# Kernel tuning notes

Measured on AMD Instinct MI355X. Metric: run time of the kernel, lower is better.

## Reference

```python
import jax, jax.numpy as jnp
import numpy as np

N = 131072      # points (rays x samples chunk)
E = 8           # spatial sub-networks (centroids)
DIN = 90        # encoded pos+dir features fed to sub-NeRFs (xyz_real=True -> x[:, 3:])
H = 256         # sub-NeRF hidden width
DOUT = 4        # rgb + sigma
MARGIN = 2.0    # boundary_margin
EPS = 1e-8


def setup_inputs() -> dict:
    key = jax.random.key(0)
    k = jax.random.split(key, 5)
    x_xyz = jax.random.uniform(k[0], (N, 3), dtype=jnp.float32)          # routing coords in [0,1)^3
    x_feat = jax.random.normal(k[1], (N, DIN), dtype=jnp.float32)        # encoded features
    x = jnp.concatenate([x_xyz, x_feat], axis=1)                         # [N, 3+DIN]
    centroids = jax.random.uniform(k[2], (E, 3), dtype=jnp.float32)
    W1 = jax.random.normal(k[3], (E, DIN, H), dtype=jnp.float32) * 0.05
    b1 = jnp.zeros((E, H), dtype=jnp.float32)
    W2 = jax.random.normal(k[4], (E, H, DOUT), dtype=jnp.float32) * 0.05
    b2 = jnp.zeros((E, DOUT), dtype=jnp.float32)
    return {"x": x, "centroids": centroids, "W1": W1, "b1": b1, "W2": W2, "b2": b2}


def reference(x, centroids, W1, b1, W2, b2):
    # --- centroid routing (torch.cdist equivalent) ---
    xyz = x[:, :3]                                                       # [N,3]
    d2 = jnp.sum((xyz[:, None, :] - centroids[None, :, :]) ** 2, axis=-1)
    dist = jnp.sqrt(jnp.maximum(d2, 0.0))                                # [N,E]
    inv = 1.0 / (dist + EPS)
    min_d = jnp.min(dist, axis=1, keepdims=True)                         # [N,1]
    inv = jnp.where(dist > MARGIN * min_d, 0.0, inv)                     # zero far experts
    weights = inv / jnp.sum(inv, axis=-1, keepdims=True)                 # [N,E], rows sum to 1

    # --- per-expert sub-NeRF MLP, weighted combine ---
    # Dense-equivalent of masked gather + weighted scatter-add: experts whose
    # weight is exactly 0 contribute nothing, matching the torch masked path.
    feat = x[:, 3:]                                                      # xyz_real=True -> drop xyz
    h = jax.nn.relu(jnp.einsum('nd,edh->enh', feat, W1) + b1[:, None, :])  # [E,N,H]
    out_e = jnp.einsum('enh,eho->eno', h, W2) + b2[:, None, :]             # [E,N,DOUT]
    return jnp.einsum('eno,ne->no', out_e, weights)                        # [N,DOUT]
```

## Files before the change

### kernel.cpp

```cpp
#include <hip/hip_runtime.h>

#define NPTS 131072
#define NE 8
#define DIN 90
#define NH 256

typedef __attribute__((ext_vector_type(8))) short bf16x8;
typedef __attribute__((ext_vector_type(4))) float f32x4;
typedef __attribute__((ext_vector_type(2))) float f32x2;
typedef __attribute__((ext_vector_type(4))) unsigned int u32x4;
typedef __attribute__((ext_vector_type(2))) unsigned int u32x2;
typedef __attribute__((ext_vector_type(4), aligned(4))) float f32x4a;
typedef __attribute__((ext_vector_type(2), aligned(4))) float f32x2a;

__device__ __forceinline__ unsigned short f2bf(float f) {
  unsigned int u = __float_as_uint(f);
  u += 0x7fffu + ((u >> 16) & 1u);
  return (unsigned short)(u >> 16);
}

#if defined(__has_builtin) && __has_builtin(__builtin_amdgcn_cvt_pk_bf16_f32)
typedef __attribute__((ext_vector_type(2))) __bf16 bf16x2;
__device__ __forceinline__ unsigned int pkbf(float f0, float f1) {
  bf16x2 r = __builtin_amdgcn_cvt_pk_bf16_f32(f0, f1);
  return __builtin_bit_cast(unsigned int, r);
}
#else
__device__ __forceinline__ unsigned int pkbf(float f0, float f1) {
  unsigned int u0 = __float_as_uint(f0) + 0x7fffu;
  unsigned int u1 = __float_as_uint(f1) + 0x7fffu;
  return __builtin_amdgcn_perm(u1, u0, 0x07060302u);
}
#endif

__device__ __forceinline__ bf16x8 cvt8(f32x4 a, f32x4 b) {
  u32x4 r;
  r[0] = pkbf(a[0], a[1]);
  r[1] = pkbf(a[2], a[3]);
  r[2] = pkbf(b[0], b[1]);
  r[3] = pkbf(b[2], b[3]);
  return __builtin_bit_cast(bf16x8, r);
}

__global__ __launch_bounds__(256) void prep(const float* __restrict__ W1,
                                            const float* __restrict__ W2,
                                            unsigned short* __restrict__ W1T,
                                            unsigned short* __restrict__ W2T) {
  const int t = threadIdx.x;
  if (blockIdx.x < 32) {
    const int e = blockIdx.x >> 2;
    const int n0 = (blockIdx.x & 3) * 64;
    __shared__ unsigned int ld[64][49];
    const int nl = t & 63;
    const int kq = t >> 6;
#pragma unroll
    for (int j = 0; j < 12; ++j) {
      const int kp2 = kq + 4 * j;
      const int k0 = 2 * kp2, k1 = k0 + 1;
      unsigned int lo = 0, hi = 0;
      if (k0 < DIN) lo = f2bf(W1[((size_t)e * DIN + k0) * NH + n0 + nl]);
      if (k1 < DIN) hi = f2bf(W1[((size_t)e * DIN + k1) * NH + n0 + nl]);
      ld[nl][kp2] = lo | (hi << 16);
    }
    __syncthreads();
    unsigned int* dst = (unsigned int*)(W1T + (size_t)(e * NH + n0) * 96);
#pragma unroll
    for (int j = 0; j < 12; ++j) {
      const int u = t + 256 * j;
      dst[u] = ld[u / 48][u % 48];
    }
  } else {
    const int e = blockIdx.x - 32;
    unsigned int* dst = (unsigned int*)W2T + (size_t)e * 2048;
    const float* src = W2 + (size_t)e * 1024;
#pragma unroll
    for (int j = 0; j < 8; ++j) {
      const int u = t + 256 * j;
      const int o = u >> 7;
      const int kp = u & 127;
      unsigned int v = 0;
      if (o < 4) {
        unsigned int lo = f2bf(src[(2 * kp) * 4 + o]);
        unsigned int hi = f2bf(src[(2 * kp + 1) * 4 + o]);
        v = lo | (hi << 16);
      }
      dst[u] = v;
    }
  }
}

__global__ __launch_bounds__(256, 3) void meganerf_main(
    const float* __restrict__ x, const float* __restrict__ cent,
    const float* __restrict__ b1, const float* __restrict__ b2,
    const unsigned short* __restrict__ W1T, const unsigned short* __restrict__ W2T,
    float* __restrict__ out) {
  __shared__ unsigned short sH[4 * 2048];
  __shared__ float sW[NE][64];
  __shared__ float sB2[64][4];
  __shared__ float sB1[NE * NH];

  const int t    = threadIdx.x;
  const int lane = t & 63;
  const int wid  = t >> 6;
  const int l15  = lane & 15;
  const int l4   = lane >> 4;
  const int row0 = blockIdx.x * 64;
  const int gbase = wid * 2048;

#pragma unroll
  for (int j = 0; j < 2; ++j)
    *(f32x4*)&sB1[t * 4 + j * 1024] = *(const f32x4a*)&b1[t * 4 + j * 1024];

  bf16x8 bfr[4][3];
#pragma unroll
  for (int nf = 0; nf < 4; ++nf) {
    const float* gr = x + (size_t)(row0 + 16 * nf + l15) * 93 + 3;
    f32x4 v0, v1;
    v0 = *(const f32x4a*)(gr + 8 * l4);
    v1 = *(const f32x4a*)(gr + 8 * l4 + 4);
    bfr[nf][0] = cvt8(v0, v1);
    v0 = *(const f32x4a*)(gr + 32 + 8 * l4);
    v1 = *(const f32x4a*)(gr + 36 + 8 * l4);
    bfr[nf][1] = cvt8(v0, v1);
    if (l4 < 3) {
      v0 = *(const f32x4a*)(gr + 64 + 8 * l4);
      v1 = *(const f32x4a*)(gr + 68 + 8 * l4);
    } else {
      f32x2 tl = *(const f32x2a*)(gr + 88);
      v0[0] = tl[0]; v0[1] = tl[1]; v0[2] = 0.f; v0[3] = 0.f;
      v1[0] = 0.f; v1[1] = 0.f; v1[2] = 0.f; v1[3] = 0.f;
    }
    bfr[nf][2] = cvt8(v0, v1);
  }

  if (t < 64) {
    const float* gx = x + (size_t)(row0 + t) * 93;
    float px = gx[0], py = gx[1], pz = gx[2];
    float dist[NE], inv[NE];
    float mind = 3.4e38f;
#pragma unroll
    for (int e = 0; e < NE; ++e) {
      float dx = px - cent[e * 3 + 0];
      float dy = py - cent[e * 3 + 1];
      float dz = pz - cent[e * 3 + 2];
      float d2 = dx * dx + dy * dy + dz * dz;
      float d = sqrtf(fmaxf(d2, 0.f));
      dist[e] = d;
      inv[e] = 1.f / (d + 1e-8f);
      mind = fminf(mind, d);
    }
    float s = 0.f;
#pragma unroll
    for (int e = 0; e < NE; ++e) {
      if (dist[e] > 2.0f * mind) inv[e] = 0.f;
      s += inv[e];
    }
    float rs = 1.f / s;
    float bb[4] = {0.f, 0.f, 0.f, 0.f};
#pragma unroll
    for (int e = 0; e < NE; ++e) {
      float w = inv[e] * rs;
      sW[e][t] = w;
#pragma unroll
      for (int o = 0; o < 4; ++o) bb[o] += w * b2[e * 4 + o];
    }
#pragma unroll
    for (int o = 0; o < 4; ++o) sB2[t][o] = bb[o];
  }
  __syncthreads();

  bf16x8 w1buf[2][6];
  bf16x8 bwbuf[2];
  float wv[4];

  auto loadW1 = [&](int idx, int buf) {
    const int e = idx >> 1, c = idx & 1;
    const unsigned short* p =
        W1T + (size_t)(e * NH + 128 * c + 32 * wid + l15) * 96 + 8 * l4;
#pragma unroll
    for (int mf = 0; mf < 2; ++mf)
#pragma unroll
      for (int ks = 0; ks < 3; ++ks)
        w1buf[buf][mf * 3 + ks] = *(const bf16x8*)(p + mf * (16 * 96) + 32 * ks);
  };
  auto loadBW = [&](int idx, int buf) {
    const int e = idx >> 1, c = idx & 1;
    bwbuf[buf] = *(const bf16x8*)(W2T + (size_t)(e * 16 + l15) * NH +
                                  128 * c + 32 * wid + 8 * l4);
  };

  loadBW(0, 0);
  loadW1(0, 0);

  f32x4 facc[4] = {{0.f, 0.f, 0.f, 0.f}, {0.f, 0.f, 0.f, 0.f},
                   {0.f, 0.f, 0.f, 0.f}, {0.f, 0.f, 0.f, 0.f}};

#pragma unroll 2
  for (int i = 0; i < 16; ++i) {
    const int e = i >> 1, c = i & 1, cur = i & 1, nxt = cur ^ 1;
    const int colbase = 128 * c + 32 * wid;

    f32x4 b1v0 = *(const f32x4*)&sB1[e * NH + colbase + 4 * l4];
    f32x4 b1v1 = *(const f32x4*)&sB1[e * NH + colbase + 16 + 4 * l4];
    if (c == 0) {
#pragma unroll
      for (int nf = 0; nf < 4; ++nf) wv[nf] = sW[e][16 * nf + l15];
    }

    const int ip = (i + 1) & 15;
    loadBW(ip, nxt);
    loadW1(ip, nxt);

#pragma unroll
    for (int mf = 0; mf < 2; ++mf) {
      const f32x4 b1v = (mf == 0) ? b1v0 : b1v1;
      f32x4 acc[4];
      __builtin_amdgcn_s_setprio(1);
#pragma unroll
      for (int nf = 0; nf < 4; ++nf)
        acc[nf] = __builtin_amdgcn_mfma_f32_16x16x32_bf16(
            w1buf[cur][mf * 3 + 0], bfr[nf][0], b1v, 0, 0, 0);
#pragma unroll
      for (int ks = 1; ks < 3; ++ks)
#pragma unroll
        for (int nf = 0; nf < 4; ++nf)
          acc[nf] = __builtin_amdgcn_mfma_f32_16x16x32_bf16(
              w1buf[cur][mf * 3 + ks], bfr[nf][ks], acc[nf], 0, 0, 0);
      __builtin_amdgcn_s_setprio(0);

#pragma unroll
      for (int nf = 0; nf < 4; ++nf) {
        const float w = wv[nf];
        f32x4 a = acc[nf];
        f32x2 p0, p1;
        p0[0] = a[0]; p0[1] = a[1];
        p1[0] = a[2]; p1[1] = a[3];
        const f32x2 z = {0.f, 0.f};
        p0 = __builtin_elementwise_max(p0, z) * w;
        p1 = __builtin_elementwise_max(p1, z) * w;
        u32x2 pk;
        pk[0] = pkbf(p0[0], p0[1]);
        pk[1] = pkbf(p1[0], p1[1]);
        *(u32x2*)&sH[gbase + (nf * 64 + (l15 + 16 * (2 * mf + (l4 >> 1)))) * 8 +
                     4 * (l4 & 1)] = pk;
      }
    }

    __builtin_amdgcn_s_setprio(1);
#pragma unroll
    for (int rf = 0; rf < 4; ++rf) {
      bf16x8 ah = *(const bf16x8*)&sH[gbase + (rf * 64 + lane) * 8];
      facc[rf] = __builtin_amdgcn_mfma_f32_16x16x32_bf16(ah, bwbuf[cur], facc[rf], 0, 0, 0);
    }
    __builtin_amdgcn_s_setprio(0);
  }

  __syncthreads();
  float* sOutP = (float*)sH;
  if (l15 < 4) {
#pragma unroll
    for (int rf = 0; rf < 4; ++rf)
#pragma unroll
      for (int r = 0; r < 4; ++r)
        sOutP[(wid * 64 + 16 * rf + 4 * l4 + r) * 4 + l15] = facc[rf][r];
  }
  __syncthreads();
  {
    const int row = t >> 2, o = t & 3;
    float v = sB2[row][o] + sOutP[(0 * 64 + row) * 4 + o] + sOutP[(1 * 64 + row) * 4 + o] +
              sOutP[(2 * 64 + row) * 4 + o] + sOutP[(3 * 64 + row) * 4 + o];
    out[row0 * 4 + t] = v;
  }
}

extern "C" void kernel_launch(void* const* d_in, const int* in_sizes, int n_in,
                              void* d_out, int out_size, void* d_ws, size_t ws_size,
                              hipStream_t stream) {
  const float* x    = (const float*)d_in[0];
  const float* cent = (const float*)d_in[1];
  const float* W1   = (const float*)d_in[2];
  const float* b1   = (const float*)d_in[3];
  const float* W2   = (const float*)d_in[4];
  const float* b2   = (const float*)d_in[5];
  float* out = (float*)d_out;

  unsigned short* W1T = (unsigned short*)d_ws;
  unsigned short* W2T = W1T + NE * NH * 96;

  prep<<<40, 256, 0, stream>>>(W1, W2, W1T, W2T);
  meganerf_main<<<NPTS / 64, 256, 0, stream>>>(x, cent, b1, b2, W1T, W2T, out);
}
```

Before: 163.5 us.

## Bucket points by active-expert mask and skip inactive experts in cooperative kernel

Adds a single cooperative persistent kernel. It converts the weights, builds a histogram of points by their routing mask, scans it, and scatters the points into a permutation grouped by mask. Each 64-point tile then runs the MLP only for the experts active in its mask, where the old kernel computed all 8 experts for every point. The cost is four grid-wide syncs, extra routing passes, gather/scatter of rows through indices, and padded partial tiles per mask bucket. The old two-kernel path stays as a fallback.

```diff
diff --git a/kernel.cpp b/kernel.cpp
--- a/kernel.cpp
+++ b/kernel.cpp
@@ -1,9 +1,13 @@
 #include <hip/hip_runtime.h>
+#include <hip/hip_cooperative_groups.h>
 
 #define NPTS 131072
 #define NE 8
 #define DIN 90
 #define NH 256
+#define NGMAX 2304
+
+namespace cg = cooperative_groups;
 
 typedef __attribute__((ext_vector_type(8))) short bf16x8;
 typedef __attribute__((ext_vector_type(4))) float f32x4;
@@ -13,6 +17,16 @@
 typedef __attribute__((ext_vector_type(4), aligned(4))) float f32x4a;
 typedef __attribute__((ext_vector_type(2), aligned(4))) float f32x2a;
 
+#define WS_W1T   0
+#define WS_W2T   393216
+#define WS_PERM  458752
+#define WS_BKTB  983040
+#define WS_HIST  984064
+#define WS_CUR   985088
+#define WS_GTB   986112
+#define WS_GTM   995328
+#define WS_END   1004544
+
 __device__ __forceinline__ unsigned short f2bf(float f) {
   unsigned int u = __float_as_uint(f);
   u += 0x7fffu + ((u >> 16) & 1u);
@@ -40,6 +54,367 @@
   r[2] = pkbf(b[0], b[1]);
   r[3] = pkbf(b[2], b[3]);
   return __builtin_bit_cast(bf16x8, r);
+}
+
+__device__ __forceinline__ int pmask(const float* __restrict__ gx,
+                                     const float* __restrict__ cent) {
+  float px = gx[0], py = gx[1], pz = gx[2];
+  float d[NE];
+  float mind = 3.4e38f;
+#pragma unroll
+  for (int e = 0; e < NE; ++e) {
+    float dx = px - cent[e * 3 + 0];
+    float dy = py - cent[e * 3 + 1];
+    float dz = pz - cent[e * 3 + 2];
+    float d2 = dx * dx + dy * dy + dz * dz;
+    d[e] = sqrtf(fmaxf(d2, 0.f));
+    mind = fminf(mind, d[e]);
+  }
+  int m = 0;
+#pragma unroll
+  for (int e = 0; e < NE; ++e)
+    if (!(d[e] > 2.0f * mind)) m |= (1 << e);
+  return m;
+}
+
+__global__ __launch_bounds__(256, 3) void mega(
+    const float* __restrict__ x, const float* __restrict__ cent,
+    const float* __restrict__ b1, const float* __restrict__ b2,
+    const float* __restrict__ W1, const float* __restrict__ W2,
+    float* __restrict__ out,
+    unsigned short* __restrict__ W1T, unsigned short* __restrict__ W2T,
+    int* __restrict__ perm, int* __restrict__ hist, int* __restrict__ cursor,
+    int* __restrict__ bktb, int* __restrict__ gt_base, int* __restrict__ gt_meta) {
+  cg::grid_group gg = cg::this_grid();
+  const int t   = threadIdx.x;
+  const int blk = blockIdx.x;
+
+  __shared__ unsigned short sH[4 * 2048];
+  __shared__ float sW[NE][64];
+  __shared__ float sB2[64][4];
+  __shared__ float sB1[NE * NH];
+  __shared__ int sIdx[64];
+  __shared__ int sElist[9];
+
+  int* lds_i = (int*)sB1;
+
+  if (blk == 0) {
+    hist[t] = 0;
+    cursor[t] = 0;
+  } else if (blk <= 32) {
+    const int e = (blk - 1) >> 2;
+    const int n0 = ((blk - 1) & 3) * 64;
+    unsigned int* ld = (unsigned int*)sH;
+    const int nl = t & 63;
+    const int kq = t >> 6;
+#pragma unroll
+    for (int j = 0; j < 12; ++j) {
+      const int kp2 = kq + 4 * j;
+      const int k0 = 2 * kp2, k1 = k0 + 1;
+      unsigned int lo = 0, hi = 0;
+      if (k0 < DIN) lo = f2bf(W1[((size_t)e * DIN + k0) * NH + n0 + nl]);
+      if (k1 < DIN) hi = f2bf(W1[((size_t)e * DIN + k1) * NH + n0 + nl]);
+      ld[nl * 49 + kp2] = lo | (hi << 16);
+    }
+    __syncthreads();
+    unsigned int* dst = (unsigned int*)(W1T + (size_t)(e * NH + n0) * 96);
+#pragma unroll
+    for (int j = 0; j < 12; ++j) {
+      const int u = t + 256 * j;
+      dst[u] = ld[(u / 48) * 49 + (u % 48)];
+    }
+  } else if (blk <= 40) {
+    const int e = blk - 33;
+    unsigned int* dst = (unsigned int*)W2T + (size_t)e * 2048;
+    const float* src = W2 + (size_t)e * 1024;
+#pragma unroll
+    for (int j = 0; j < 8; ++j) {
+      const int u = t + 256 * j;
+      const int o = u >> 7, kp = u & 127;
+      unsigned int v = 0;
+      if (o < 4) {
+        unsigned int lo = f2bf(src[(2 * kp) * 4 + o]);
+        unsigned int hi = f2bf(src[(2 * kp + 1) * 4 + o]);
+        v = lo | (hi << 16);
+      }
+      dst[u] = v;
+    }
+  }
+  gg.sync();
+
+  if (blk < 128) {
+    int* lhist = lds_i;
+    lhist[t] = 0;
+    __syncthreads();
+#pragma unroll
+    for (int j = 0; j < 4; ++j) {
+      const int p = blk * 1024 + j * 256 + t;
+      const int m = pmask(x + (size_t)p * 93, cent);
+      atomicAdd(&lhist[m], 1);
+    }
+    __syncthreads();
+    if (lhist[t] > 0) atomicAdd(&hist[t], lhist[t]);
+  }
+  gg.sync();
+
+  if (blk == 0) {
+    int* s1 = lds_i;
+    int* s2 = lds_i + 256;
+    const int c = hist[t];
+    s1[t] = c;
+    __syncthreads();
+    for (int off = 1; off < 256; off <<= 1) {
+      int a = s1[t];
+      int bb = (t >= off) ? s1[t - off] : 0;
+      __syncthreads();
+      s1[t] = a + bb;
+      __syncthreads();
+    }
+    const int base = s1[t] - c;
+    bktb[t] = base;
+    const int gc = (c + 63) >> 6;
+    s2[t] = gc;
+    __syncthreads();
+    for (int off = 1; off < 256; off <<= 1) {
+      int a = s2[t];
+      int bb = (t >= off) ? s2[t - off] : 0;
+      __syncthreads();
+      s2[t] = a + bb;
+      __syncthreads();
+    }
+    const int goff = s2[t] - gc;
+    for (int j = 0; j < gc; ++j) {
+      const int rem = c - 64 * j;
+      gt_base[goff + j] = base + 64 * j;
+      gt_meta[goff + j] = t | ((rem < 64 ? rem : 64) << 8);
+    }
+    __syncthreads();
+    const int total = s2[255];
+    for (int s = total + t; s < NGMAX; s += 256) gt_meta[s] = 0;
+  }
+  gg.sync();
+
+  if (blk < 128) {
+    int* lhist = lds_i;
+    int* lbase = lds_i + 256;
+    int* lcur  = lds_i + 512;
+    lhist[t] = 0;
+    lcur[t] = 0;
+    __syncthreads();
+    int msk[4];
+#pragma unroll
+    for (int j = 0; j < 4; ++j) {
+      const int p = blk * 1024 + j * 256 + t;
+      msk[j] = pmask(x + (size_t)p * 93, cent);
+      atomicAdd(&lhist[msk[j]], 1);
+    }
+    __syncthreads();
+    if (lhist[t] > 0) lbase[t] = bktb[t] + atomicAdd(&cursor[t], lhist[t]);
+    __syncthreads();
+#pragma unroll
+    for (int j = 0; j < 4; ++j) {
+      const int p = blk * 1024 + j * 256 + t;
+      const int lp = atomicAdd(&lcur[msk[j]], 1);
+      perm[lbase[msk[j]] + lp] = p;
+    }
+  }
+  gg.sync();
+
+  const int lane = t & 63;
+  const int wid  = t >> 6;
+  const int l15  = lane & 15;
+  const int l4   = lane >> 4;
+  const int hb   = wid * 2048;
+
+#pragma unroll
+  for (int j = 0; j < 2; ++j)
+    *(f32x4*)&sB1[t * 4 + j * 1024] = *(const f32x4a*)&b1[t * 4 + j * 1024];
+
+  for (int g = blk; g < NGMAX; g += gridDim.x) {
+    const int meta = gt_meta[g];
+    const int cnt = meta >> 8;
+    if (cnt == 0) continue;
+    const int gmask = meta & 255;
+    const int base = gt_base[g];
+
+    __syncthreads();
+    if (t < 64) sIdx[t] = perm[base + (t < cnt ? t : cnt - 1)];
+    if (t == 0) {
+      int ne = 0;
+#pragma unroll
+      for (int e = 0; e < NE; ++e)
+        if ((gmask >> e) & 1) sElist[ne++] = e;
+      sElist[8] = ne;
+    }
+    __syncthreads();
+
+    bf16x8 bfr[4][3];
+#pragma unroll
+    for (int nf = 0; nf < 4; ++nf) {
+      const float* gr = x + (size_t)sIdx[16 * nf + l15] * 93 + 3;
+      f32x4 v0, v1;
+      v0 = *(const f32x4a*)(gr + 8 * l4);
+      v1 = *(const f32x4a*)(gr + 8 * l4 + 4);
+      bfr[nf][0] = cvt8(v0, v1);
+      v0 = *(const f32x4a*)(gr + 32 + 8 * l4);
+      v1 = *(const f32x4a*)(gr + 36 + 8 * l4);
+      bfr[nf][1] = cvt8(v0, v1);
+      if (l4 < 3) {
+        v0 = *(const f32x4a*)(gr + 64 + 8 * l4);
+        v1 = *(const f32x4a*)(gr + 68 + 8 * l4);
+      } else {
+        f32x2 tl = *(const f32x2a*)(gr + 88);
+        v0[0] = tl[0]; v0[1] = tl[1]; v0[2] = 0.f; v0[3] = 0.f;
+        v1[0] = 0.f; v1[1] = 0.f; v1[2] = 0.f; v1[3] = 0.f;
+      }
+      bfr[nf][2] = cvt8(v0, v1);
+    }
+
+    if (t < 64) {
+      const float* gx = x + (size_t)sIdx[t] * 93;
+      float px = gx[0], py = gx[1], pz = gx[2];
+      float dist[NE], inv[NE];
+      float mind = 3.4e38f;
+#pragma unroll
+      for (int e = 0; e < NE; ++e) {
+        float dx = px - cent[e * 3 + 0];
+        float dy = py - cent[e * 3 + 1];
+        float dz = pz - cent[e * 3 + 2];
+        float d2 = dx * dx + dy * dy + dz * dz;
+        float d = sqrtf(fmaxf(d2, 0.f));
+        dist[e] = d;
+        inv[e] = 1.f / (d + 1e-8f);
+        mind = fminf(mind, d);
+      }
+      float s = 0.f;
+#pragma unroll
+      for (int e = 0; e < NE; ++e) {
+        if (dist[e] > 2.0f * mind) inv[e] = 0.f;
+        s += inv[e];
+      }
+      float rs = 1.f / s;
+      float bb[4] = {0.f, 0.f, 0.f, 0.f};
+#pragma unroll
+      for (int e = 0; e < NE; ++e) {
+        float w = inv[e] * rs;
+        sW[e][t] = w;
+#pragma unroll
+        for (int o = 0; o < 4; ++o) bb[o] += w * b2[e * 4 + o];
+      }
+#pragma unroll
+      for (int o = 0; o < 4; ++o) sB2[t][o] = bb[o];
+    }
+    __syncthreads();
+
+    const int ne = sElist[8];
+    const int niter = 2 * ne;
+
+    bf16x8 w1A[6], w1B[6], bwA, bwB;
+    float wv[4];
+    f32x4 facc[4] = {{0.f, 0.f, 0.f, 0.f}, {0.f, 0.f, 0.f, 0.f},
+                     {0.f, 0.f, 0.f, 0.f}, {0.f, 0.f, 0.f, 0.f}};
+
+    auto loadW1 = [&](int e, int c, bf16x8 (&dst)[6]) {
+      const unsigned short* p =
+          W1T + (size_t)(e * NH + 128 * c + 32 * wid + l15) * 96 + 8 * l4;
+#pragma unroll
+      for (int mf = 0; mf < 2; ++mf)
+#pragma unroll
+        for (int ks = 0; ks < 3; ++ks)
+          dst[mf * 3 + ks] = *(const bf16x8*)(p + mf * (16 * 96) + 32 * ks);
+    };
+    auto loadBW = [&](int e, int c, bf16x8& dst) {
+      dst = *(const bf16x8*)(W2T + (size_t)(e * 16 + l15) * NH +
+                             128 * c + 32 * wid + 8 * l4);
+    };
+
+    auto body = [&](int e, int c, int ep, int cp, bool ldwv,
+                    bf16x8 (&wcur)[6], bf16x8& bwcur,
+                    bf16x8 (&wnxt)[6], bf16x8& bwnxt) {
+      const int colbase = 128 * c + 32 * wid;
+      f32x4 b1v0 = *(const f32x4*)&sB1[e * NH + colbase + 4 * l4];
+      f32x4 b1v1 = *(const f32x4*)&sB1[e * NH + colbase + 16 + 4 * l4];
+      if (ldwv) {
+#pragma unroll
+        for (int nf = 0; nf < 4; ++nf) wv[nf] = sW[e][16 * nf + l15];
+      }
+      loadBW(ep, cp, bwnxt);
+      loadW1(ep, cp, wnxt);
+#pragma unroll
+      for (int mf = 0; mf < 2; ++mf) {
+        const f32x4 b1v = (mf == 0) ? b1v0 : b1v1;
+        f32x4 acc[4];
+        __builtin_amdgcn_s_setprio(1);
+#pragma unroll
+        for (int nf = 0; nf < 4; ++nf)
+          acc[nf] = __builtin_amdgcn_mfma_f32_16x16x32_bf16(
+              wcur[mf * 3 + 0], bfr[nf][0], b1v, 0, 0, 0);
+#pragma unroll
+        for (int ks = 1; ks < 3; ++ks)
+#pragma unroll
+          for (int nf = 0; nf < 4; ++nf)
+            acc[nf] = __builtin_amdgcn_mfma_f32_16x16x32_bf16(
+                wcur[mf * 3 + ks], bfr[nf][ks], acc[nf], 0, 0, 0);
+        __builtin_amdgcn_s_setprio(0);
+#pragma unroll
+        for (int nf = 0; nf < 4; ++nf) {
+          const float w = wv[nf];
+          f32x4 a = acc[nf];
+          f32x2 p0, p1;
+          p0[0] = a[0]; p0[1] = a[1];
+          p1[0] = a[2]; p1[1] = a[3];
+          const f32x2 z = {0.f, 0.f};
+          p0 = __builtin_elementwise_max(p0, z) * w;
+          p1 = __builtin_elementwise_max(p1, z) * w;
+          u32x2 pk;
+          pk[0] = pkbf(p0[0], p0[1]);
+          pk[1] = pkbf(p1[0], p1[1]);
+          *(u32x2*)&sH[hb + (nf * 64 + (l15 + 16 * (2 * mf + (l4 >> 1)))) * 8 +
+                       4 * (l4 & 1)] = pk;
+        }
+      }
+      __builtin_amdgcn_s_setprio(1);
+#pragma unroll
+      for (int rf = 0; rf < 4; ++rf) {
+        bf16x8 ah = *(const bf16x8*)&sH[hb + (rf * 64 + lane) * 8];
+        facc[rf] =
+            __builtin_amdgcn_mfma_f32_16x16x32_bf16(ah, bwcur, facc[rf], 0, 0, 0);
+      }
+      __builtin_amdgcn_s_setprio(0);
+    };
+
+    loadBW(sElist[0], 0, bwA);
+    loadW1(sElist[0], 0, w1A);
+
+    for (int i = 0; i < niter; i += 2) {
+      const int e = sElist[i >> 1];
+      const int ip2 = (i + 2 < niter) ? i + 2 : i + 1;
+      const int e2 = sElist[ip2 >> 1];
+      const int c2 = ip2 & 1;
+      body(e, 0, e, 1, true, w1A, bwA, w1B, bwB);
+      body(e, 1, e2, c2, false, w1B, bwB, w1A, bwA);
+    }
+
+    __syncthreads();
+    float* sOutP = (float*)sH;
+    if (l15 < 4) {
+#pragma unroll
+      for (int rf = 0; rf < 4; ++rf)
+#pragma unroll
+        for (int r = 0; r < 4; ++r)
+          sOutP[(wid * 64 + 16 * rf + 4 * l4 + r) * 4 + l15] = facc[rf][r];
+    }
+    __syncthreads();
+    {
+      const int row = t >> 2, o = t & 3;
+      if (row < cnt) {
+        float v = sB2[row][o] + sOutP[(0 * 64 + row) * 4 + o] +
+                  sOutP[(1 * 64 + row) * 4 + o] + sOutP[(2 * 64 + row) * 4 + o] +
+                  sOutP[(3 * 64 + row) * 4 + o];
+        out[(size_t)sIdx[row] * 4 + o] = v;
+      }
+    }
+  }
 }
 
 __global__ __launch_bounds__(256) void prep(const float* __restrict__ W1,
@@ -199,18 +574,15 @@
   for (int i = 0; i < 16; ++i) {
     const int e = i >> 1, c = i & 1, cur = i & 1, nxt = cur ^ 1;
     const int colbase = 128 * c + 32 * wid;
-
     f32x4 b1v0 = *(const f32x4*)&sB1[e * NH + colbase + 4 * l4];
     f32x4 b1v1 = *(const f32x4*)&sB1[e * NH + colbase + 16 + 4 * l4];
     if (c == 0) {
 #pragma unroll
       for (int nf = 0; nf < 4; ++nf) wv[nf] = sW[e][16 * nf + l15];
     }
-
     const int ip = (i + 1) & 15;
     loadBW(ip, nxt);
     loadW1(ip, nxt);
-
 #pragma unroll
     for (int mf = 0; mf < 2; ++mf) {
       const f32x4 b1v = (mf == 0) ? b1v0 : b1v1;
@@ -227,7 +599,6 @@
           acc[nf] = __builtin_amdgcn_mfma_f32_16x16x32_bf16(
               w1buf[cur][mf * 3 + ks], bfr[nf][ks], acc[nf], 0, 0, 0);
       __builtin_amdgcn_s_setprio(0);
-
 #pragma unroll
       for (int nf = 0; nf < 4; ++nf) {
         const float w = wv[nf];
@@ -245,7 +616,6 @@
                      4 * (l4 & 1)] = pk;
       }
     }
-
     __builtin_amdgcn_s_setprio(1);
 #pragma unroll
     for (int rf = 0; rf < 4; ++rf) {
@@ -284,9 +654,41 @@
   const float* b2   = (const float*)d_in[5];
   float* out = (float*)d_out;
 
-  unsigned short* W1T = (unsigned short*)d_ws;
-  unsigned short* W2T = W1T + NE * NH * 96;
-
-  prep<<<40, 256, 0, stream>>>(W1, W2, W1T, W2T);
-  meganerf_main<<<NPTS / 64, 256, 0, stream>>>(x, cent, b1, b2, W1T, W2T, out);
-}
+  char* ws = (char*)d_ws;
+  unsigned short* W1T = (unsigned short*)(ws + WS_W1T);
+  unsigned short* W2T = (unsigned short*)(ws + WS_W2T);
+  int* perm   = (int*)(ws + WS_PERM);
+  int* bktb   = (int*)(ws + WS_BKTB);
+  int* hist   = (int*)(ws + WS_HIST);
+  int* cursor = (int*)(ws + WS_CUR);
+  int* gtb    = (int*)(ws + WS_GTB);
+  int* gtm    = (int*)(ws + WS_GTM);
+
+  static int nblk = -2;
+  if (nblk == -2) {
+    int bpc = 0;
+    if (hipOccupancyMaxActiveBlocksPerMultiprocessor(&bpc, mega, 256, 0) ==
+            hipSuccess && bpc > 0) {
+      long nb = (long)bpc * 256;
+      nblk = nb > NGMAX ? NGMAX : (int)nb;
+    } else {
+      nblk = -1;
+    }
+  }
+
+  bool ok = false;
+  if (nblk >= 128 && ws_size >= (size_t)WS_END) {
+    const float *xa = x, *ca = cent, *b1a = b1, *b2a = b2, *W1a = W1, *W2a = W2;
+    float* oa = out;
+    unsigned short *w1t = W1T, *w2t = W2T;
+    int *pm = perm, *hh = hist, *cu = cursor, *bb = bktb, *g1 = gtb, *g2 = gtm;
+    void* args[] = {&xa, &ca, &b1a, &b2a, &W1a, &W2a, &oa,
+                    &w1t, &w2t, &pm, &hh, &cu, &bb, &g1, &g2};
+    ok = hipLaunchCooperativeKernel(mega, dim3(nblk), dim3(256), args, 0,
+                                    stream) == hipSuccess;
+  }
+  if (!ok) {
+    prep<<<40, 256, 0, stream>>>(W1, W2, W1T, W2T);
+    meganerf_main<<<NPTS / 64, 256, 0, stream>>>(x, cent, b1, b2, W1T, W2T, out);
+  }
+}
```

Measured after the change: 321.2 us. 1.96x slower.

## Bucket points by active-expert mask and run MLP only for active experts

Applied to the files above, without the earlier changes.

Adds a routing pre-pass that computes each point's active-expert bitmask, builds a histogram, prefix-scans it into 64-point tiles per mask, and scatters point indices into a permutation. The main kernel then gathers points per tile and loops only over the experts present in that tile's mask, skipping MLP work for experts with zero weight. This trades several extra small launches, atomics and indirect gathered loads for fewer MFMA iterations. The inner loop is also restructured into explicitly double-buffered macro steps with named registers.

```diff
diff --git a/kernel.cpp b/kernel.cpp
--- a/kernel.cpp
+++ b/kernel.cpp
@@ -4,6 +4,7 @@
 #define NE 8
 #define DIN 90
 #define NH 256
+#define NGMAX 2304
 
 typedef __attribute__((ext_vector_type(8))) short bf16x8;
 typedef __attribute__((ext_vector_type(4))) float f32x4;
@@ -13,6 +14,16 @@
 typedef __attribute__((ext_vector_type(4), aligned(4))) float f32x4a;
 typedef __attribute__((ext_vector_type(2), aligned(4))) float f32x2a;
 
+#define WS_W1T   0
+#define WS_W2T   393216
+#define WS_PERM  458752
+#define WS_BKTB  983040
+#define WS_HIST  984064
+#define WS_CUR   985088
+#define WS_GTB   986112
+#define WS_GTM   995328
+#define WS_END   1004544
+
 __device__ __forceinline__ unsigned short f2bf(float f) {
   unsigned int u = __float_as_uint(f);
   u += 0x7fffu + ((u >> 16) & 1u);
@@ -42,15 +53,42 @@
   return __builtin_bit_cast(bf16x8, r);
 }
 
-__global__ __launch_bounds__(256) void prep(const float* __restrict__ W1,
-                                            const float* __restrict__ W2,
-                                            unsigned short* __restrict__ W1T,
-                                            unsigned short* __restrict__ W2T) {
+__device__ __forceinline__ int pmask(const float* __restrict__ gx,
+                                     const float* __restrict__ cent) {
+  float px = gx[0], py = gx[1], pz = gx[2];
+  float d[NE];
+  float mind = 3.4e38f;
+#pragma unroll
+  for (int e = 0; e < NE; ++e) {
+    float dx = px - cent[e * 3 + 0];
+    float dy = py - cent[e * 3 + 1];
+    float dz = pz - cent[e * 3 + 2];
+    float d2 = dx * dx + dy * dy + dz * dz;
+    d[e] = sqrtf(fmaxf(d2, 0.f));
+    mind = fminf(mind, d[e]);
+  }
+  int m = 0;
+#pragma unroll
+  for (int e = 0; e < NE; ++e)
+    if (!(d[e] > 2.0f * mind)) m |= (1 << e);
+  return m;
+}
+
+__global__ __launch_bounds__(512) void zerok(int* __restrict__ p) {
+  p[threadIdx.x] = 0;
+}
+
+__global__ __launch_bounds__(256) void prep_mask(
+    const float* __restrict__ W1, const float* __restrict__ W2,
+    const float* __restrict__ x, const float* __restrict__ cent,
+    unsigned short* __restrict__ W1T, unsigned short* __restrict__ W2T,
+    int* __restrict__ hist) {
   const int t = threadIdx.x;
-  if (blockIdx.x < 32) {
-    const int e = blockIdx.x >> 2;
-    const int n0 = (blockIdx.x & 3) * 64;
-    __shared__ unsigned int ld[64][49];
+  const int blk = blockIdx.x;
+  __shared__ unsigned int shm[64 * 49];
+  if (blk < 32) {
+    const int e = blk >> 2;
+    const int n0 = (blk & 3) * 64;
     const int nl = t & 63;
     const int kq = t >> 6;
 #pragma unroll
@@ -60,24 +98,23 @@
       unsigned int lo = 0, hi = 0;
       if (k0 < DIN) lo = f2bf(W1[((size_t)e * DIN + k0) * NH + n0 + nl]);
       if (k1 < DIN) hi = f2bf(W1[((size_t)e * DIN + k1) * NH + n0 + nl]);
-      ld[nl][kp2] = lo | (hi << 16);
+      shm[nl * 49 + kp2] = lo | (hi << 16);
     }
     __syncthreads();
     unsigned int* dst = (unsigned int*)(W1T + (size_t)(e * NH + n0) * 96);
 #pragma unroll
     for (int j = 0; j < 12; ++j) {
       const int u = t + 256 * j;
-      dst[u] = ld[u / 48][u % 48];
-    }
-  } else {
-    const int e = blockIdx.x - 32;
+      dst[u] = shm[(u / 48) * 49 + (u % 48)];
+    }
+  } else if (blk < 40) {
+    const int e = blk - 32;
     unsigned int* dst = (unsigned int*)W2T + (size_t)e * 2048;
     const float* src = W2 + (size_t)e * 1024;
 #pragma unroll
     for (int j = 0; j < 8; ++j) {
       const int u = t + 256 * j;
-      const int o = u >> 7;
-      const int kp = u & 127;
+      const int o = u >> 7, kp = u & 127;
       unsigned int v = 0;
       if (o < 4) {
         unsigned int lo = f2bf(src[(2 * kp) * 4 + o]);
@@ -85,6 +122,313 @@
         v = lo | (hi << 16);
       }
       dst[u] = v;
+    }
+  } else {
+    int* lh = (int*)shm;
+    lh[t] = 0;
+    __syncthreads();
+    const int base = (blk - 40) * 1024;
+#pragma unroll
+    for (int j = 0; j < 4; ++j) {
+      const int m = pmask(x + (size_t)(base + j * 256 + t) * 93, cent);
+      atomicAdd(&lh[m], 1);
+    }
+    __syncthreads();
+    if (lh[t] > 0) atomicAdd(&hist[t], lh[t]);
+  }
+}
+
+__global__ __launch_bounds__(256) void scank(const int* __restrict__ hist,
+                                             int* __restrict__ bktb,
+                                             int* __restrict__ gt_base,
+                                             int* __restrict__ gt_meta) {
+  __shared__ int s1[256], s2[256];
+  const int t = threadIdx.x;
+  const int c = hist[t];
+  s1[t] = c;
+  __syncthreads();
+  for (int off = 1; off < 256; off <<= 1) {
+    int a = s1[t];
+    int b = (t >= off) ? s1[t - off] : 0;
+    __syncthreads();
+    s1[t] = a + b;
+    __syncthreads();
+  }
+  const int base = s1[t] - c;
+  bktb[t] = base;
+  const int gc = (c + 63) >> 6;
+  s2[t] = gc;
+  __syncthreads();
+  for (int off = 1; off < 256; off <<= 1) {
+    int a = s2[t];
+    int b = (t >= off) ? s2[t - off] : 0;
+    __syncthreads();
+    s2[t] = a + b;
+    __syncthreads();
+  }
+  const int goff = s2[t] - gc;
+  for (int j = 0; j < gc; ++j) {
+    const int rem = c - 64 * j;
+    gt_base[goff + j] = base + 64 * j;
+    gt_meta[goff + j] = t | ((rem < 64 ? rem : 64) << 8);
+  }
+  __syncthreads();
+  const int total = s2[255];
+  for (int s = total + t; s < NGMAX; s += 256) gt_meta[s] = 0;
+}
+
+__global__ __launch_bounds__(256) void scatterk(const float* __restrict__ x,
+                                                const float* __restrict__ cent,
+                                                const int* __restrict__ bktb,
+                                                int* __restrict__ cursor,
+                                                int* __restrict__ perm) {
+  __shared__ int lh[256], lb[256], lc[256];
+  const int t = threadIdx.x;
+  lh[t] = 0;
+  lc[t] = 0;
+  __syncthreads();
+  const int base = blockIdx.x * 1024;
+  int m[4];
+#pragma unroll
+  for (int j = 0; j < 4; ++j) {
+    m[j] = pmask(x + (size_t)(base + j * 256 + t) * 93, cent);
+    atomicAdd(&lh[m[j]], 1);
+  }
+  __syncthreads();
+  if (lh[t] > 0) lb[t] = bktb[t] + atomicAdd(&cursor[t], lh[t]);
+  __syncthreads();
+#pragma unroll
+  for (int j = 0; j < 4; ++j) {
+    const int p = base + j * 256 + t;
+    const int lp = atomicAdd(&lc[m[j]], 1);
+    perm[lb[m[j]] + lp] = p;
+  }
+}
+
+#define UNRL _Pragma("unroll")
+
+#define LOADW1(E_, C_, D0, D1, D2, D3, D4, D5)                                  \
+  do {                                                                          \
+    const unsigned short* _p =                                                  \
+        W1T + (size_t)((E_) * NH + 128 * (C_) + 32 * wid + l15) * 96 + 8 * l4;  \
+    D0 = *(const bf16x8*)(_p);                                                  \
+    D1 = *(const bf16x8*)(_p + 32);                                             \
+    D2 = *(const bf16x8*)(_p + 64);                                             \
+    D3 = *(const bf16x8*)(_p + 1536);                                           \
+    D4 = *(const bf16x8*)(_p + 1568);                                           \
+    D5 = *(const bf16x8*)(_p + 1600);                                           \
+  } while (0)
+
+#define LOADBW(E_, C_, D)                                                       \
+  do {                                                                          \
+    D = *(const bf16x8*)(W2T + (size_t)((E_) * 16 + l15) * NH + 128 * (C_) +    \
+                         32 * wid + 8 * l4);                                    \
+  } while (0)
+
+#define EPI(MF)                                                                 \
+  UNRL for (int nf = 0; nf < 4; ++nf) {                                         \
+    const float _w = wv[nf];                                                    \
+    f32x4 _a = acc[nf];                                                         \
+    f32x2 _p0, _p1;                                                             \
+    _p0[0] = _a[0]; _p0[1] = _a[1];                                             \
+    _p1[0] = _a[2]; _p1[1] = _a[3];                                             \
+    const f32x2 _z = {0.f, 0.f};                                                \
+    _p0 = __builtin_elementwise_max(_p0, _z) * _w;                              \
+    _p1 = __builtin_elementwise_max(_p1, _z) * _w;                              \
+    u32x2 _pk;                                                                  \
+    _pk[0] = pkbf(_p0[0], _p0[1]);                                              \
+    _pk[1] = pkbf(_p1[0], _p1[1]);                                              \
+    *(u32x2*)&sH[gbase + (nf * 64 + (l15 + 16 * (2 * (MF) + (l4 >> 1)))) * 8 +  \
+                 4 * (l4 & 1)] = _pk;                                           \
+  }
+
+#define STEP(E_, C_, LDWV_, EP_, CP_, CW0, CW1, CW2, CW3, CW4, CW5, CBW,        \
+             NW0, NW1, NW2, NW3, NW4, NW5, NBW)                                 \
+  do {                                                                          \
+    const int _cb = 128 * (C_) + 32 * wid;                                      \
+    f32x4 _b1v0 = *(const f32x4*)&sB1[(E_) * NH + _cb + 4 * l4];                \
+    f32x4 _b1v1 = *(const f32x4*)&sB1[(E_) * NH + _cb + 16 + 4 * l4];           \
+    if (LDWV_) {                                                                \
+      UNRL for (int nf = 0; nf < 4; ++nf) wv[nf] = sW[(E_)][16 * nf + l15];     \
+    }                                                                           \
+    LOADBW(EP_, CP_, NBW);                                                      \
+    LOADW1(EP_, CP_, NW0, NW1, NW2, NW3, NW4, NW5);                             \
+    {                                                                           \
+      f32x4 acc[4];                                                             \
+      __builtin_amdgcn_s_setprio(1);                                            \
+      UNRL for (int nf = 0; nf < 4; ++nf)                                       \
+          acc[nf] = __builtin_amdgcn_mfma_f32_16x16x32_bf16(CW0, bfr[nf][0],    \
+                                                            _b1v0, 0, 0, 0);    \
+      UNRL for (int nf = 0; nf < 4; ++nf)                                       \
+          acc[nf] = __builtin_amdgcn_mfma_f32_16x16x32_bf16(CW1, bfr[nf][1],    \
+                                                            acc[nf], 0, 0, 0);  \
+      UNRL for (int nf = 0; nf < 4; ++nf)                                       \
+          acc[nf] = __builtin_amdgcn_mfma_f32_16x16x32_bf16(CW2, bfr[nf][2],    \
+                                                            acc[nf], 0, 0, 0);  \
+      __builtin_amdgcn_s_setprio(0);                                            \
+      EPI(0)                                                                    \
+      __builtin_amdgcn_s_setprio(1);                                            \
+      UNRL for (int nf = 0; nf < 4; ++nf)                                       \
+          acc[nf] = __builtin_amdgcn_mfma_f32_16x16x32_bf16(CW3, bfr[nf][0],    \
+                                                            _b1v1, 0, 0, 0);    \
+      UNRL for (int nf = 0; nf < 4; ++nf)                                       \
+          acc[nf] = __builtin_amdgcn_mfma_f32_16x16x32_bf16(CW4, bfr[nf][1],    \
+                                                            acc[nf], 0, 0, 0);  \
+      UNRL for (int nf = 0; nf < 4; ++nf)                                       \
+          acc[nf] = __builtin_amdgcn_mfma_f32_16x16x32_bf16(CW5, bfr[nf][2],    \
+                                                            acc[nf], 0, 0, 0);  \
+      __builtin_amdgcn_s_setprio(0);                                            \
+      EPI(1)                                                                    \
+    }                                                                           \
+    __builtin_amdgcn_s_setprio(1);                                              \
+    UNRL for (int rf = 0; rf < 4; ++rf) {                                       \
+      bf16x8 _ah = *(const bf16x8*)&sH[gbase + (rf * 64 + lane) * 8];           \
+      facc[rf] = __builtin_amdgcn_mfma_f32_16x16x32_bf16(_ah, CBW, facc[rf],    \
+                                                         0, 0, 0);              \
+    }                                                                           \
+    __builtin_amdgcn_s_setprio(0);                                              \
+  } while (0)
+
+__global__ __launch_bounds__(256, 3) void main_sparse(
+    const float* __restrict__ x, const float* __restrict__ cent,
+    const float* __restrict__ b1, const float* __restrict__ b2,
+    const unsigned short* __restrict__ W1T, const unsigned short* __restrict__ W2T,
+    const int* __restrict__ perm, const int* __restrict__ gt_base,
+    const int* __restrict__ gt_meta, float* __restrict__ out) {
+  const int meta = gt_meta[blockIdx.x];
+  const int cnt = meta >> 8;
+  if (cnt == 0) return;
+  const int gmask = meta & 255;
+  const int base = gt_base[blockIdx.x];
+
+  __shared__ unsigned short sH[4 * 2048];
+  __shared__ float sW[NE][64];
+  __shared__ float sB2[64][4];
+  __shared__ float sB1[NE * NH];
+  __shared__ int sIdx[64];
+  __shared__ int sElist[9];
+
+  const int t    = threadIdx.x;
+  const int lane = t & 63;
+  const int wid  = t >> 6;
+  const int l15  = lane & 15;
+  const int l4   = lane >> 4;
+  const int gbase = wid * 2048;
+
+#pragma unroll
+  for (int j = 0; j < 2; ++j)
+    *(f32x4*)&sB1[t * 4 + j * 1024] = *(const f32x4a*)&b1[t * 4 + j * 1024];
+  if (t < 64) sIdx[t] = perm[base + (t < cnt ? t : cnt - 1)];
+  if (t == 0) {
+    int ne = 0;
+#pragma unroll
+    for (int e = 0; e < NE; ++e)
+      if ((gmask >> e) & 1) sElist[ne++] = e;
+    sElist[8] = ne;
+  }
+  __syncthreads();
+
+  bf16x8 bfr[4][3];
+#pragma unroll
+  for (int nf = 0; nf < 4; ++nf) {
+    const float* gr = x + (size_t)sIdx[16 * nf + l15] * 93 + 3;
+    f32x4 v0, v1;
+    v0 = *(const f32x4a*)(gr + 8 * l4);
+    v1 = *(const f32x4a*)(gr + 8 * l4 + 4);
+    bfr[nf][0] = cvt8(v0, v1);
+    v0 = *(const f32x4a*)(gr + 32 + 8 * l4);
+    v1 = *(const f32x4a*)(gr + 36 + 8 * l4);
+    bfr[nf][1] = cvt8(v0, v1);
+    if (l4 < 3) {
+      v0 = *(const f32x4a*)(gr + 64 + 8 * l4);
+      v1 = *(const f32x4a*)(gr + 68 + 8 * l4);
+    } else {
+      f32x2 tl = *(const f32x2a*)(gr + 88);
+      v0[0] = tl[0]; v0[1] = tl[1]; v0[2] = 0.f; v0[3] = 0.f;
+      v1[0] = 0.f; v1[1] = 0.f; v1[2] = 0.f; v1[3] = 0.f;
+    }
+    bfr[nf][2] = cvt8(v0, v1);
+  }
+
+  if (t < 64) {
+    const float* gx = x + (size_t)sIdx[t] * 93;
+    float px = gx[0], py = gx[1], pz = gx[2];
+    float dist[NE], inv[NE];
+    float mind = 3.4e38f;
+#pragma unroll
+    for (int e = 0; e < NE; ++e) {
+      float dx = px - cent[e * 3 + 0];
+      float dy = py - cent[e * 3 + 1];
+      float dz = pz - cent[e * 3 + 2];
+      float d2 = dx * dx + dy * dy + dz * dz;
+      float d = sqrtf(fmaxf(d2, 0.f));
+      dist[e] = d;
+      inv[e] = 1.f / (d + 1e-8f);
+      mind = fminf(mind, d);
+    }
+    float s = 0.f;
+#pragma unroll
+    for (int e = 0; e < NE; ++e) {
+      if (dist[e] > 2.0f * mind) inv[e] = 0.f;
+      s += inv[e];
+    }
+    float rs = 1.f / s;
+    float bb[4] = {0.f, 0.f, 0.f, 0.f};
+#pragma unroll
+    for (int e = 0; e < NE; ++e) {
+      float w = inv[e] * rs;
+      sW[e][t] = w;
+#pragma unroll
+      for (int o = 0; o < 4; ++o) bb[o] += w * b2[e * 4 + o];
+    }
+#pragma unroll
+    for (int o = 0; o < 4; ++o) sB2[t][o] = bb[o];
+  }
+  __syncthreads();
+
+  const int niter = 2 * sElist[8];
+
+  bf16x8 w1A0, w1A1, w1A2, w1A3, w1A4, w1A5;
+  bf16x8 w1B0, w1B1, w1B2, w1B3, w1B4, w1B5;
+  bf16x8 bwA, bwB;
+  float wv[4];
+  f32x4 facc[4] = {{0.f, 0.f, 0.f, 0.f}, {0.f, 0.f, 0.f, 0.f},
+                   {0.f, 0.f, 0.f, 0.f}, {0.f, 0.f, 0.f, 0.f}};
+
+  {
+    const int e0 = sElist[0];
+    LOADBW(e0, 0, bwA);
+    LOADW1(e0, 0, w1A0, w1A1, w1A2, w1A3, w1A4, w1A5);
+  }
+
+  for (int i = 0; i < niter; i += 2) {
+    const int e = sElist[i >> 1];
+    const int ip2 = (i + 2 < niter) ? (i + 2) : (i + 1);
+    const int e2 = sElist[ip2 >> 1];
+    const int c2 = ip2 & 1;
+    STEP(e, 0, 1, e, 1, w1A0, w1A1, w1A2, w1A3, w1A4, w1A5, bwA,
+         w1B0, w1B1, w1B2, w1B3, w1B4, w1B5, bwB);
+    STEP(e, 1, 0, e2, c2, w1B0, w1B1, w1B2, w1B3, w1B4, w1B5, bwB,
+         w1A0, w1A1, w1A2, w1A3, w1A4, w1A5, bwA);
+  }
+
+  __syncthreads();
+  float* sOutP = (float*)sH;
+  if (l15 < 4) {
+#pragma unroll
+    for (int rf = 0; rf < 4; ++rf)
+#pragma unroll
+      for (int r = 0; r < 4; ++r)
+        sOutP[(wid * 64 + 16 * rf + 4 * l4 + r) * 4 + l15] = facc[rf][r];
+  }
+  __syncthreads();
+  {
+    const int row = t >> 2, o = t & 3;
+    if (row < cnt) {
+      float v = sB2[row][o] + sOutP[(0 * 64 + row) * 4 + o] +
+                sOutP[(1 * 64 + row) * 4 + o] + sOutP[(2 * 64 + row) * 4 + o] +
+                sOutP[(3 * 64 + row) * 4 + o];
+      out[(size_t)sIdx[row] * 4 + o] = v;
     }
   }
 }
@@ -169,90 +513,24 @@
   }
   __syncthreads();
 
-  bf16x8 w1buf[2][6];
-  bf16x8 bwbuf[2];
+  bf16x8 w1A0, w1A1, w1A2, w1A3, w1A4, w1A5;
+  bf16x8 w1B0, w1B1, w1B2, w1B3, w1B4, w1B5;
+  bf16x8 bwA, bwB;
   float wv[4];
-
-  auto loadW1 = [&](int idx, int buf) {
-    const int e = idx >> 1, c = idx & 1;
-    const unsigned short* p =
-        W1T + (size_t)(e * NH + 128 * c + 32 * wid + l15) * 96 + 8 * l4;
-#pragma unroll
-    for (int mf = 0; mf < 2; ++mf)
-#pragma unroll
-      for (int ks = 0; ks < 3; ++ks)
-        w1buf[buf][mf * 3 + ks] = *(const bf16x8*)(p + mf * (16 * 96) + 32 * ks);
-  };
-  auto loadBW = [&](int idx, int buf) {
-    const int e = idx >> 1, c = idx & 1;
-    bwbuf[buf] = *(const bf16x8*)(W2T + (size_t)(e * 16 + l15) * NH +
-                                  128 * c + 32 * wid + 8 * l4);
-  };
-
-  loadBW(0, 0);
-  loadW1(0, 0);
-
   f32x4 facc[4] = {{0.f, 0.f, 0.f, 0.f}, {0.f, 0.f, 0.f, 0.f},
                    {0.f, 0.f, 0.f, 0.f}, {0.f, 0.f, 0.f, 0.f}};
 
-#pragma unroll 2
-  for (int i = 0; i < 16; ++i) {
-    const int e = i >> 1, c = i & 1, cur = i & 1, nxt = cur ^ 1;
-    const int colbase = 128 * c + 32 * wid;
-
-    f32x4 b1v0 = *(const f32x4*)&sB1[e * NH + colbase + 4 * l4];
-    f32x4 b1v1 = *(const f32x4*)&sB1[e * NH + colbase + 16 + 4 * l4];
-    if (c == 0) {
-#pragma unroll
-      for (int nf = 0; nf < 4; ++nf) wv[nf] = sW[e][16 * nf + l15];
-    }
-
-    const int ip = (i + 1) & 15;
-    loadBW(ip, nxt);
-    loadW1(ip, nxt);
-
-#pragma unroll
-    for (int mf = 0; mf < 2; ++mf) {
-      const f32x4 b1v = (mf == 0) ? b1v0 : b1v1;
-      f32x4 acc[4];
-      __builtin_amdgcn_s_setprio(1);
-#pragma unroll
-      for (int nf = 0; nf < 4; ++nf)
-        acc[nf] = __builtin_amdgcn_mfma_f32_16x16x32_bf16(
-            w1buf[cur][mf * 3 + 0], bfr[nf][0], b1v, 0, 0, 0);
-#pragma unroll
-      for (int ks = 1; ks < 3; ++ks)
-#pragma unroll
-        for (int nf = 0; nf < 4; ++nf)
-          acc[nf] = __builtin_amdgcn_mfma_f32_16x16x32_bf16(
-              w1buf[cur][mf * 3 + ks], bfr[nf][ks], acc[nf], 0, 0, 0);
-      __builtin_amdgcn_s_setprio(0);
-
-#pragma unroll
-      for (int nf = 0; nf < 4; ++nf) {
-        const float w = wv[nf];
-        f32x4 a = acc[nf];
-        f32x2 p0, p1;
-        p0[0] = a[0]; p0[1] = a[1];
-        p1[0] = a[2]; p1[1] = a[3];
-        const f32x2 z = {0.f, 0.f};
-        p0 = __builtin_elementwise_max(p0, z) * w;
-        p1 = __builtin_elementwise_max(p1, z) * w;
-        u32x2 pk;
-        pk[0] = pkbf(p0[0], p0[1]);
-        pk[1] = pkbf(p1[0], p1[1]);
-        *(u32x2*)&sH[gbase + (nf * 64 + (l15 + 16 * (2 * mf + (l4 >> 1)))) * 8 +
-                     4 * (l4 & 1)] = pk;
-      }
-    }
-
-    __builtin_amdgcn_s_setprio(1);
-#pragma unroll
-    for (int rf = 0; rf < 4; ++rf) {
-      bf16x8 ah = *(const bf16x8*)&sH[gbase + (rf * 64 + lane) * 8];
-      facc[rf] = __builtin_amdgcn_mfma_f32_16x16x32_bf16(ah, bwbuf[cur], facc[rf], 0, 0, 0);
-    }
-    __builtin_amdgcn_s_setprio(0);
+  LOADBW(0, 0, bwA);
+  LOADW1(0, 0, w1A0, w1A1, w1A2, w1A3, w1A4, w1A5);
+
+  for (int i = 0; i < 16; i += 2) {
+    const int e = i >> 1;
+    const int ip2 = (i + 2) & 15;
+    const int e2 = ip2 >> 1;
+    STEP(e, 0, 1, e, 1, w1A0, w1A1, w1A2, w1A3, w1A4, w1A5, bwA,
+         w1B0, w1B1, w1B2, w1B3, w1B4, w1B5, bwB);
+    STEP(e, 1, 0, e2, 0, w1B0, w1B1, w1B2, w1B3, w1B4, w1B5, bwB,
+         w1A0, w1A1, w1A2, w1A3, w1A4, w1A5, bwA);
   }
 
   __syncthreads();
@@ -284,9 +562,25 @@
   const float* b2   = (const float*)d_in[5];
   float* out = (float*)d_out;
 
-  unsigned short* W1T = (unsigned short*)d_ws;
-  unsigned short* W2T = W1T + NE * NH * 96;
-
-  prep<<<40, 256, 0, stream>>>(W1, W2, W1T, W2T);
-  meganerf_main<<<NPTS / 64, 256, 0, stream>>>(x, cent, b1, b2, W1T, W2T, out);
-}
+  char* ws = (char*)d_ws;
+  unsigned short* W1T = (unsigned short*)(ws + WS_W1T);
+  unsigned short* W2T = (unsigned short*)(ws + WS_W2T);
+  int* perm   = (int*)(ws + WS_PERM);
+  int* bktb   = (int*)(ws + WS_BKTB);
+  int* hist   = (int*)(ws + WS_HIST);
+  int* cursor = (int*)(ws + WS_CUR);
+  int* gtb    = (int*)(ws + WS_GTB);
+  int* gtm    = (int*)(ws + WS_GTM);
+
+  if (ws_size >= (size_t)WS_END) {
+    zerok<<<1, 512, 0, stream>>>(hist);
+    prep_mask<<<168, 256, 0, stream>>>(W1, W2, x, cent, W1T, W2T, hist);
+    scank<<<1, 256, 0, stream>>>(hist, bktb, gtb, gtm);
+    scatterk<<<128, 256, 0, stream>>>(x, cent, bktb, cursor, perm);
+    main_sparse<<<NGMAX, 256, 0, stream>>>(x, cent, b1, b2, W1T, W2T, perm, gtb,
+                                           gtm, out);
+  } else {
+    prep_mask<<<40, 256, 0, stream>>>(W1, W2, x, cent, W1T, W2T, hist);
+    meganerf_main<<<NPTS / 64, 256, 0, stream>>>(x, cent, b1, b2, W1T, W2T, out);
+  }
+}
```

After: 173.3 us. 1.06x slower.
